# Kernel optimization log

Hardware: AMD Instinct MI355X
Metric: run time of the kernel (lower is better)

The kernel has to match this reference:

```python
import jax, jax.numpy as jnp
import numpy as np
import math

CH = 256
GROUPS = max(min(CH // 4, 32), 1)  # default_num_groups -> 32
EPS = 1e-5


def group_norm(x, gamma, beta):
    # x: [B, C, H, W]
    B, C, H, W = x.shape
    xg = x.reshape(B, GROUPS, C // GROUPS, H, W)
    mu = jnp.mean(xg, axis=(2, 3, 4), keepdims=True)
    var = jnp.var(xg, axis=(2, 3, 4), keepdims=True)
    xn = ((xg - mu) * jax.lax.rsqrt(var + EPS)).reshape(B, C, H, W)
    return xn * gamma[None, :, None, None] + beta[None, :, None, None]


def conv1x1(x, w, b):
    # x: [B, C_in, H, W]; w: [C_out, C_in]; b: [C_out]
    return jnp.einsum('oc,bchw->bohw', w, x) + b[None, :, None, None]


def xavier(key, shape, gain):
    fan_in, fan_out = shape[1], shape[0]
    limit = gain * math.sqrt(6.0 / (fan_in + fan_out))
    return jax.random.uniform(key, shape, jnp.float32, -limit, limit)


def setup_inputs() -> dict:
    key = jax.random.key(0)
    ks = jax.random.split(key, 6)
    x = jax.random.normal(ks[0], (32, CH, 32, 32), jnp.float32)
    gamma = jnp.ones((CH,), jnp.float32)
    beta = jnp.zeros((CH,), jnp.float32)
    g = math.sqrt(0.1)  # init_scale=0.1 for q,k,v
    wq = xavier(ks[1], (CH, CH), g)
    wk = xavier(ks[2], (CH, CH), g)
    wv = xavier(ks[3], (CH, CH), g)
    # w_h uses init_scale=0.0 -> zeros in original; use small nonzero so output is exercised
    wh = xavier(ks[4], (CH, CH), 0.1)
    bq = jnp.zeros((CH,), jnp.float32)
    bk = jnp.zeros((CH,), jnp.float32)
    bv = jnp.zeros((CH,), jnp.float32)
    bh = jnp.zeros((CH,), jnp.float32)
    return dict(x=x, gamma=gamma, beta=beta, wq=wq, bq=bq, wk=wk, bk=bk,
                wv=wv, bv=bv, wh=wh, bh=bh)


def reference(x, gamma, beta, wq, bq, wk, bk, wv, bv, wh, bh):
    B, C, H, W = x.shape
    N = H * W
    h = group_norm(x, gamma, beta)
    q = conv1x1(h, wq, bq).reshape(B, C, N)
    k = conv1x1(h, wk, bk).reshape(B, C, N)
    v = conv1x1(h, wv, bv).reshape(B, C, N)
    # full attention over spatial tokens: scores [B, N, N]
    scores = jnp.einsum('bcn,bcm->bnm', q, k) / math.sqrt(C)
    attn = jax.nn.softmax(scores, axis=-1)
    h = jnp.einsum('bnm,bcm->bcn', attn, v).reshape(B, C, H, W)
    h = conv1x1(h, wh, bh)
    return x + h  # skip_rescale=False
```

## Files before the change

kernel.cpp:

```cpp
#include <hip/hip_runtime.h>

typedef __bf16 bf16_t;
typedef __bf16 bf16x8 __attribute__((ext_vector_type(8)));
typedef __bf16 bf16x4 __attribute__((ext_vector_type(4)));
typedef float f32x4 __attribute__((ext_vector_type(4)));
typedef float f32x16 __attribute__((ext_vector_type(16)));
typedef long longx2 __attribute__((ext_vector_type(2)));
typedef unsigned uintx2 __attribute__((ext_vector_type(2)));

static constexpr int kC = 256;
static constexpr int kN = 1024;
static constexpr int kB = 32;

__device__ __forceinline__ void gload_lds16(const void* g, void* l) {
  __builtin_amdgcn_global_load_lds(
      (const __attribute__((address_space(1))) unsigned int*)g,
      (__attribute__((address_space(3))) unsigned int*)l, 16, 0, 0);
}

__device__ __forceinline__ unsigned pk_fp8x4(float a, float b, float c, float d) {
  unsigned r;
  asm("v_cvt_pk_fp8_f32 %0, %1, %2" : "=v"(r) : "v"(a), "v"(b));
  asm("v_cvt_pk_fp8_f32 %0, %1, %2 op_sel:[0,0,1]" : "+v"(r) : "v"(c), "v"(d));
  return r;
}

__device__ __forceinline__ void pl32swap(unsigned& a, unsigned& b) {
  asm("v_permlane32_swap_b32 %0, %1" : "+v"(a), "+v"(b));
}

__device__ __forceinline__ float cross_half_sum(float rs) {
  unsigned a = __builtin_bit_cast(unsigned, rs), b = a;
  pl32swap(a, b);
  return __builtin_bit_cast(float, a) + __builtin_bit_cast(float, b);
}

__global__ __launch_bounds__(256) void gn_castw_k(const float* __restrict__ x,
                                                  const float* __restrict__ gamma,
                                                  const float* __restrict__ beta,
                                                  bf16_t* __restrict__ hn,
                                                  const float* __restrict__ wq,
                                                  const float* __restrict__ wk,
                                                  const float* __restrict__ wv,
                                                  const float* __restrict__ wh,
                                                  bf16_t* __restrict__ wb) {
  __shared__ float xs[8 * 1040];
  __shared__ float red[8];
  __shared__ float stat[2];
  int t = threadIdx.x;
  if (blockIdx.x >= 1024) {
    int i = (blockIdx.x - 1024) * 256 + t;
    wb[i] = (bf16_t)wq[i];
    wb[i + 65536] = (bf16_t)wk[i];
    wb[i + 131072] = (bf16_t)wv[i];
    wb[i + 196608] = (bf16_t)wh[i];
    return;
  }
  int bg = blockIdx.x;
  int b = bg >> 5, g = bg & 31;
  const float* base = x + (size_t)bg * 8192;
  float s = 0.f, q = 0.f;
#pragma unroll
  for (int i = 0; i < 8; ++i) {
    float4 v = *(const float4*)(base + i * 1024 + t * 4);
    *(float4*)(xs + i * 1040 + t * 4) = v;
    s += v.x + v.y + v.z + v.w;
    q += v.x * v.x + v.y * v.y + v.z * v.z + v.w * v.w;
  }
#pragma unroll
  for (int o = 32; o; o >>= 1) { s += __shfl_down(s, o); q += __shfl_down(q, o); }
  int w = t >> 6;
  if ((t & 63) == 0) { red[w] = s; red[4 + w] = q; }
  __syncthreads();
  if (t == 0) {
    float S = red[0] + red[1] + red[2] + red[3];
    float Q = red[4] + red[5] + red[6] + red[7];
    float mean = S * (1.f / 8192.f);
    float var = Q * (1.f / 8192.f) - mean * mean;
    stat[0] = mean;
    stat[1] = rsqrtf(var + 1e-5f);
  }
  __syncthreads();
  float mean = stat[0], rstd = stat[1];
  float gmb[8], btb[8];
#pragma unroll
  for (int j = 0; j < 8; ++j) { gmb[j] = gamma[g * 8 + j]; btb[j] = beta[g * 8 + j]; }
  bf16_t* hb = hn + (size_t)b * (kN * kC) + g * 8;
#pragma unroll
  for (int i = 0; i < 4; ++i) {
    int n = i * 256 + t;
    bf16x8 o;
#pragma unroll
    for (int j = 0; j < 8; ++j)
      o[j] = (bf16_t)((xs[j * 1040 + n] - mean) * rstd * gmb[j] + btb[j]);
    *(bf16x8*)(hb + (size_t)n * kC) = o;
  }
}

__global__ __launch_bounds__(256, 2) void fattn_k(const char* __restrict__ QT,
                                                  const char* __restrict__ KT,
                                                  const char* __restrict__ VV,
                                                  bf16_t* __restrict__ OT) {
  __shared__ char smem[70656];
  char* lKc = smem;
  char* lVc = smem + 32768;
  char* pb = smem + 65536;
  float* exls = (float*)(smem + 69632);
  int t = threadIdx.x;
  int wid = t >> 6, lane = t & 63;
  int l31 = lane & 31, hi = lane >> 5;
  int qg = wid & 1, h = wid >> 1;
  int bid = blockIdx.x;
  int b = ((bid & 7) << 2) | ((bid >> 3) & 3);
  int qt = bid >> 5;
  const char* Qb = QT + (size_t)b * (kN * kC);
  int q0 = qt * 64 + qg * 32;
  constexpr float kSc = 0.0625f * 1.44269504f;

  long qf[16];
#pragma unroll
  for (int jj = 0; jj < 8; ++jj) {
    longx2 qp = *(const longx2*)(Qb + (size_t)(q0 + l31) * kC + hi * 128 + jj * 16);
    qf[2 * jj] = qp[0];
    qf[2 * jj + 1] = qp[1];
  }

  unsigned koff2[8];
#pragma unroll
  for (int jj = 0; jj < 8; ++jj)
    koff2[jj] = (h * 32 + l31) * 256 + (((hi * 8 + jj) ^ (l31 & 15)) << 4);
  unsigned voff2[8];
#pragma unroll
  for (int sp = 0; sp < 2; ++sp)
#pragma unroll
    for (int ct = 0; ct < 4; ++ct) {
      int c = h * 128 + ct * 32 + l31;
      voff2[sp * 4 + ct] = c * 64 + ((sp ^ ((c >> 1) & 1)) << 5) + hi * 16;
    }

  unsigned koffg[4], voffg[4];
#pragma unroll
  for (int i = 0; i < 4; ++i) {
    int ck = i * 256 + t;
    int row = ck >> 4, s = ck & 15;
    koffg[i] = row * 256 + ((s ^ (row & 15)) << 4);
    int cv = i * 256 + t;
    voffg[i] = (cv >> 2) * 1024 + ((cv & 3) << 4);
  }
  const char* kSrc = KT + (size_t)b * (kN * kC);
  const char* vSrc = VV + (size_t)b * (kC * kN);
  char* kd0 = lKc + t * 16;
  char* vd0 = lVc + t * 16;

  f32x16 acc[4] = {};
  float lsum = 0.f;

  auto STAGE = [&](int buf) {
#pragma unroll
    for (int i = 0; i < 4; ++i)
      gload_lds16(kSrc + koffg[i], kd0 + buf * 16384 + i * 4096);
#pragma unroll
    for (int i = 0; i < 4; ++i)
      gload_lds16(vSrc + voffg[i], vd0 + buf * 16384 + i * 4096);
    kSrc += 16384;
    vSrc += 64;
  };

  STAGE(0);
  for (int kt = 0; kt < 16; ++kt) {
    if (kt < 15) {
      STAGE((kt + 1) & 1);
      asm volatile("s_waitcnt vmcnt(8)" ::: "memory");
    } else {
      asm volatile("s_waitcnt vmcnt(0)" ::: "memory");
    }
    __builtin_amdgcn_s_barrier();
    const char* bK = lKc + (kt & 1) * 16384;
    const char* bV = lVc + (kt & 1) * 16384;
    f32x16 sa = {};
    __builtin_amdgcn_s_setprio(1);
#pragma unroll
    for (int jj = 0; jj < 8; ++jj) {
      longx2 ka = *(const longx2*)(bK + koff2[jj]);
      sa = __builtin_amdgcn_mfma_f32_32x32x16_fp8_fp8(ka[0], qf[2 * jj], sa, 0, 0, 0);
      sa = __builtin_amdgcn_mfma_f32_32x32x16_fp8_fp8(ka[1], qf[2 * jj + 1], sa, 0, 0, 0);
    }
    __builtin_amdgcn_s_setprio(0);
    float rs = 0.f;
    float e0 = exp2f(sa[0] * kSc), e1 = exp2f(sa[1] * kSc);
    float e2 = exp2f(sa[2] * kSc), e3 = exp2f(sa[3] * kSc);
    float e4 = exp2f(sa[4] * kSc), e5 = exp2f(sa[5] * kSc);
    float e6 = exp2f(sa[6] * kSc), e7 = exp2f(sa[7] * kSc);
    rs += e0 + e1 + e2 + e3 + e4 + e5 + e6 + e7;
    unsigned G0 = pk_fp8x4(e0, e1, e2, e3), G1 = pk_fp8x4(e4, e5, e6, e7);
    pl32swap(G0, G1);
    e0 = exp2f(sa[8] * kSc);  e1 = exp2f(sa[9] * kSc);
    e2 = exp2f(sa[10] * kSc); e3 = exp2f(sa[11] * kSc);
    e4 = exp2f(sa[12] * kSc); e5 = exp2f(sa[13] * kSc);
    e6 = exp2f(sa[14] * kSc); e7 = exp2f(sa[15] * kSc);
    rs += e0 + e1 + e2 + e3 + e4 + e5 + e6 + e7;
    lsum += rs;
    unsigned G2 = pk_fp8x4(e0, e1, e2, e3), G3 = pk_fp8x4(e4, e5, e6, e7);
    pl32swap(G2, G3);
    *(uint4*)(pb + wid * 1024 + lane * 16) = make_uint4(G0, G1, G2, G3);
    asm volatile("s_waitcnt lgkmcnt(0)" ::: "memory");
    __builtin_amdgcn_s_barrier();
    uint4 po = *(const uint4*)(pb + (wid ^ 2) * 1024 + lane * 16);
    long own0 = __builtin_bit_cast(long, uintx2{G0, G1});
    long own1 = __builtin_bit_cast(long, uintx2{G2, G3});
    long pr0 = __builtin_bit_cast(long, uintx2{po.x, po.y});
    long pr1 = __builtin_bit_cast(long, uintx2{po.z, po.w});
    long s0 = h ? pr0 : own0, s1 = h ? pr1 : own1;
    long s2 = h ? own0 : pr0, s3 = h ? own1 : pr1;
    __builtin_amdgcn_s_setprio(1);
#pragma unroll
    for (int ct = 0; ct < 4; ++ct) {
      longx2 vv = *(const longx2*)(bV + voff2[ct]);
      acc[ct] = __builtin_amdgcn_mfma_f32_32x32x16_fp8_fp8(s0, vv[0], acc[ct], 0, 0, 0);
      acc[ct] = __builtin_amdgcn_mfma_f32_32x32x16_fp8_fp8(s1, vv[1], acc[ct], 0, 0, 0);
    }
#pragma unroll
    for (int ct = 0; ct < 4; ++ct) {
      longx2 vv = *(const longx2*)(bV + voff2[4 + ct]);
      acc[ct] = __builtin_amdgcn_mfma_f32_32x32x16_fp8_fp8(s2, vv[0], acc[ct], 0, 0, 0);
      acc[ct] = __builtin_amdgcn_mfma_f32_32x32x16_fp8_fp8(s3, vv[1], acc[ct], 0, 0, 0);
    }
    __builtin_amdgcn_s_setprio(0);
    __builtin_amdgcn_s_barrier();
  }

  float ls = cross_half_sum(lsum);
  exls[wid * 64 + lane] = ls;
  __syncthreads();
  ls += exls[(wid ^ 2) * 64 + lane];
  float inv = 1.f / ls;
  float invR[16];
#pragma unroll
  for (int r = 0; r < 16; ++r)
    invR[r] = __shfl(inv, (r & 3) + 8 * (r >> 2) + 4 * hi);
  bf16_t* Ob = OT + (size_t)b * (kN * kC);
#pragma unroll
  for (int ct = 0; ct < 4; ++ct)
#pragma unroll
    for (int r = 0; r < 16; ++r) {
      int qr = (r & 3) + 8 * (r >> 2) + 4 * hi;
      Ob[(size_t)(q0 + qr) * kC + h * 128 + ct * 32 + l31] =
          (bf16_t)(acc[ct][r] * invR[r]);
    }
}

__global__ __launch_bounds__(256) void qkv_gemm_k(const bf16_t* __restrict__ W,
                                                  const bf16_t* __restrict__ HNall,
                                                  char* __restrict__ QTo,
                                                  char* __restrict__ KTo,
                                                  char* __restrict__ VVo,
                                                  const float* __restrict__ bq,
                                                  const float* __restrict__ bk,
                                                  const float* __restrict__ bv) {
  __shared__ bf16_t lA[2][128 * 64];
  __shared__ bf16_t lB[2][128 * 64];
  int bid = blockIdx.x;
  int b = bid / 48;
  int rem = bid - b * 48;
  int tmi = rem >> 3, tni = rem & 7;
  const bf16_t* Ab = W + (size_t)tmi * 128 * 256;
  const bf16_t* Bb = HNall + (size_t)b * (kN * kC) + (size_t)tni * 128 * 256;
  int t = threadIdx.x;
  int wid = t >> 6, l = t & 63;
  int wm = wid >> 1, wn = wid & 1;
  int lr = l & 15, lk = l >> 4;
  unsigned goff[4];
#pragma unroll
  for (int i = 0; i < 4; ++i) {
    int ci = i * 256 + t;
    int row = ci >> 3, s = ci & 7;
    goff[i] = row * 256 + ((s ^ (row & 7)) << 3);
  }
  unsigned aoff[8], boff[8];
#pragma unroll
  for (int kk = 0; kk < 2; ++kk)
#pragma unroll
    for (int f = 0; f < 4; ++f) {
      int ra = wm * 64 + f * 16 + lr;
      int rb2 = wn * 64 + f * 16 + lr;
      int ch = kk * 4 + lk;
      aoff[kk * 4 + f] = ra * 64 + ((ch ^ (ra & 7)) << 3);
      boff[kk * 4 + f] = rb2 * 64 + ((ch ^ (rb2 & 7)) << 3);
    }
  f32x4 acc[4][4] = {};
  auto STAGE = [&](int buf, int k0) {
#pragma unroll
    for (int i = 0; i < 4; ++i) {
      gload_lds16(Ab + k0 + goff[i], &lA[buf][t * 8 + i * 2048]);
      gload_lds16(Bb + k0 + goff[i], &lB[buf][t * 8 + i * 2048]);
    }
  };
  STAGE(0, 0);
  for (int kt = 0; kt < 4; ++kt) {
    if (kt < 3) {
      STAGE((kt + 1) & 1, (kt + 1) * 64);
      asm volatile("s_waitcnt vmcnt(8)" ::: "memory");
    } else {
      asm volatile("s_waitcnt vmcnt(0)" ::: "memory");
    }
    __builtin_amdgcn_s_barrier();
    const bf16_t* cA = lA[kt & 1];
    const bf16_t* cB = lB[kt & 1];
#pragma unroll
    for (int kk = 0; kk < 2; ++kk) {
      bf16x8 af[4], bfr[4];
#pragma unroll
      for (int f = 0; f < 4; ++f) {
        af[f] = *(const bf16x8*)(cA + aoff[kk * 4 + f]);
        bfr[f] = *(const bf16x8*)(cB + boff[kk * 4 + f]);
      }
#pragma unroll
      for (int mf = 0; mf < 4; ++mf)
#pragma unroll
        for (int nf = 0; nf < 4; ++nf)
          acc[mf][nf] = __builtin_amdgcn_mfma_f32_16x16x32_bf16(af[mf], bfr[nf],
                                                                acc[mf][nf], 0, 0, 0);
    }
    __builtin_amdgcn_s_barrier();
  }
  int seg = tmi >> 1;
  int rb = (tmi & 1) * 128 + wm * 64;
  int cb = tni * 128 + wn * 64;
  if (seg < 2) {
    char* D = (seg ? KTo : QTo) + (size_t)b * (kN * kC);
    const float* bias = seg ? bk : bq;
#pragma unroll
    for (int mf = 0; mf < 4; ++mf)
#pragma unroll
      for (int nf = 0; nf < 4; ++nf) {
        int r0 = rb + mf * 16 + lk * 4;
        int c = cb + nf * 16 + lr;
        unsigned u = pk_fp8x4(acc[mf][nf][0] + bias[r0], acc[mf][nf][1] + bias[r0 + 1],
                              acc[mf][nf][2] + bias[r0 + 2], acc[mf][nf][3] + bias[r0 + 3]);
        int np = ((r0 >> 3) & 1) * 128 + (r0 >> 4) * 8 + (r0 & 7);
        *(unsigned*)(D + (size_t)c * kC + np) = u;
      }
  } else {
    char* D = VVo + (size_t)b * (kC * kN);
#pragma unroll
    for (int mf = 0; mf < 4; ++mf)
#pragma unroll
      for (int nf = 0; nf < 4; ++nf) {
        int r0 = rb + mf * 16 + lk * 4;
        int c = cb + nf * 16 + lr;
        unsigned u = pk_fp8x4(acc[mf][nf][0] + bv[r0], acc[mf][nf][1] + bv[r0 + 1],
                              acc[mf][nf][2] + bv[r0 + 2], acc[mf][nf][3] + bv[r0 + 3]);
        int kv = c & 63, tile = c >> 6;
        int sp = kv >> 5;
        int base = tile * 64 + ((kv >> 3) & 1) * 16 + ((kv >> 4) & 1) * 8 + (kv & 7);
#pragma unroll
        for (int i = 0; i < 4; ++i) {
          int ch = r0 + i;
          int pos = base + ((sp ^ ((ch >> 1) & 1)) << 5);
          D[(size_t)ch * kN + pos] = (char)(u >> (8 * i));
        }
      }
  }
}

__global__ __launch_bounds__(256) void out_gemm_k(const bf16_t* __restrict__ A,
                                                  const bf16_t* __restrict__ BT,
                                                  float* __restrict__ Dst,
                                                  const float* __restrict__ bias,
                                                  const float* __restrict__ resid) {
  __shared__ bf16_t lA[2][128 * 64];
  __shared__ bf16_t lB[2][128 * 64];
  int bid = blockIdx.x;
  int b = bid >> 4;
  int rem = bid & 15;
  int tmi = rem >> 1, tni = rem & 1;
  const bf16_t* Ab = A + (size_t)b * (kN * kC) + (size_t)tmi * 128 * 256;
  const bf16_t* Bb = BT + (size_t)tni * 128 * 256;
  int t = threadIdx.x;
  int wid = t >> 6, l = t & 63;
  int wm = wid >> 1, wn = wid & 1;
  int lr = l & 15, lk = l >> 4;
  unsigned goff[4];
#pragma unroll
  for (int i = 0; i < 4; ++i) {
    int ci = i * 256 + t;
    int row = ci >> 3, s = ci & 7;
    goff[i] = row * 256 + ((s ^ (row & 7)) << 3);
  }
  unsigned aoff[8], boff[8];
#pragma unroll
  for (int kk = 0; kk < 2; ++kk)
#pragma unroll
    for (int f = 0; f < 4; ++f) {
      int ra = wm * 64 + f * 16 + lr;
      int rb2 = wn * 64 + f * 16 + lr;
      int ch = kk * 4 + lk;
      aoff[kk * 4 + f] = ra * 64 + ((ch ^ (ra & 7)) << 3);
      boff[kk * 4 + f] = rb2 * 64 + ((ch ^ (rb2 & 7)) << 3);
    }
  f32x4 acc[4][4] = {};
  auto STAGE = [&](int buf, int k0) {
#pragma unroll
    for (int i = 0; i < 4; ++i) {
      gload_lds16(Ab + k0 + goff[i], &lA[buf][t * 8 + i * 2048]);
      gload_lds16(Bb + k0 + goff[i], &lB[buf][t * 8 + i * 2048]);
    }
  };
  STAGE(0, 0);
  for (int kt = 0; kt < 4; ++kt) {
    if (kt < 3) {
      STAGE((kt + 1) & 1, (kt + 1) * 64);
      asm volatile("s_waitcnt vmcnt(8)" ::: "memory");
    } else {
      asm volatile("s_waitcnt vmcnt(0)" ::: "memory");
    }
    __builtin_amdgcn_s_barrier();
    const bf16_t* cA = lA[kt & 1];
    const bf16_t* cB = lB[kt & 1];
#pragma unroll
    for (int kk = 0; kk < 2; ++kk) {
      bf16x8 af[4], bfr[4];
#pragma unroll
      for (int f = 0; f < 4; ++f) {
        af[f] = *(const bf16x8*)(cA + aoff[kk * 4 + f]);
        bfr[f] = *(const bf16x8*)(cB + boff[kk * 4 + f]);
      }
#pragma unroll
      for (int mf = 0; mf < 4; ++mf)
#pragma unroll
        for (int nf = 0; nf < 4; ++nf)
          acc[mf][nf] = __builtin_amdgcn_mfma_f32_16x16x32_bf16(af[mf], bfr[nf],
                                                                acc[mf][nf], 0, 0, 0);
    }
    __builtin_amdgcn_s_barrier();
  }
  int rb = tmi * 128 + wm * 64;
  int cb = tni * 128 + wn * 64;
  float* D = Dst + (size_t)b * (kC * kN);
  const float* R = resid + (size_t)b * (kC * kN);
#pragma unroll
  for (int mf = 0; mf < 4; ++mf)
#pragma unroll
    for (int nf = 0; nf < 4; ++nf) {
      int r0 = rb + mf * 16 + lk * 4;
      int c = cb + nf * 16 + lr;
      float4 rv = *(const float4*)(R + (size_t)c * kN + r0);
      float bc = bias[c];
      float4 o2 = make_float4(acc[mf][nf][0] + rv.x + bc, acc[mf][nf][1] + rv.y + bc,
                              acc[mf][nf][2] + rv.z + bc, acc[mf][nf][3] + rv.w + bc);
      *(float4*)(D + (size_t)c * kN + r0) = o2;
    }
}

extern "C" void kernel_launch(void* const* d_in, const int* in_sizes, int n_in,
                              void* d_out, int out_size, void* d_ws, size_t ws_size,
                              hipStream_t stream) {
  (void)in_sizes; (void)n_in; (void)out_size; (void)ws_size;
  const float* x = (const float*)d_in[0];
  const float* gamma = (const float*)d_in[1];
  const float* beta = (const float*)d_in[2];
  const float* wq = (const float*)d_in[3];
  const float* bq = (const float*)d_in[4];
  const float* wk = (const float*)d_in[5];
  const float* bk = (const float*)d_in[6];
  const float* wv = (const float*)d_in[7];
  const float* bv = (const float*)d_in[8];
  const float* wh = (const float*)d_in[9];
  const float* bh = (const float*)d_in[10];
  float* out = (float*)d_out;

  char* ws = (char*)d_ws;
  bf16_t* HN = (bf16_t*)(ws);
  char* QT = ws + 16777216;
  char* KT = ws + 25165824;
  char* VV = ws + 33554432;
  bf16_t* WB = (bf16_t*)(ws + 50331648);

  gn_castw_k<<<kB * 32 + 256, 256, 0, stream>>>(x, gamma, beta, HN, wq, wk, wv, wh, WB);
  qkv_gemm_k<<<kB * 48, 256, 0, stream>>>(WB, HN, QT, KT, VV, bq, bk, bv);
  fattn_k<<<512, 256, 0, stream>>>(QT, KT, VV, HN);
  out_gemm_k<<<kB * 16, 256, 0, stream>>>(HN, WB + 196608, out, bh, x);
}
```

Baseline: 102.2 us.

## Keep activation tile resident in LDS and stream all QKV weight tiles

The QKV projection GEMM now loads a block's full 128x256 normalized-activation tile into LDS once. It then loops over all six 128-row weight tiles with double-buffered 64-wide K chunks, using 512 threads per block and 256 blocks instead of 1536. This removes the six-fold re-reading of the activation tile from global memory. The cost is a large LDS footprint (64KB plus the weight buffers), fewer blocks, and serialized epilogue stores inside the loop, which may lower occupancy and latency hiding.

```diff
diff --git a/kernel.cpp b/kernel.cpp
--- a/kernel.cpp
+++ b/kernel.cpp
@@ -249,7 +249,7 @@
     }
 }
 
-__global__ __launch_bounds__(256) void qkv_gemm_k(const bf16_t* __restrict__ W,
+__global__ __launch_bounds__(512) void qkv_gemm_k(const bf16_t* __restrict__ W,
                                                   const bf16_t* __restrict__ HNall,
                                                   char* __restrict__ QTo,
                                                   char* __restrict__ KTo,
@@ -257,109 +257,128 @@
                                                   const float* __restrict__ bq,
                                                   const float* __restrict__ bk,
                                                   const float* __restrict__ bv) {
-  __shared__ bf16_t lA[2][128 * 64];
-  __shared__ bf16_t lB[2][128 * 64];
+  __shared__ bf16_t lH[128 * 256];
+  __shared__ bf16_t lW[2][128 * 64];
   int bid = blockIdx.x;
-  int b = bid / 48;
-  int rem = bid - b * 48;
-  int tmi = rem >> 3, tni = rem & 7;
-  const bf16_t* Ab = W + (size_t)tmi * 128 * 256;
+  int b = bid >> 3, tni = bid & 7;
   const bf16_t* Bb = HNall + (size_t)b * (kN * kC) + (size_t)tni * 128 * 256;
   int t = threadIdx.x;
   int wid = t >> 6, l = t & 63;
   int wm = wid >> 1, wn = wid & 1;
   int lr = l & 15, lk = l >> 4;
-  unsigned goff[4];
-#pragma unroll
-  for (int i = 0; i < 4; ++i) {
-    int ci = i * 256 + t;
-    int row = ci >> 3, s = ci & 7;
-    goff[i] = row * 256 + ((s ^ (row & 7)) << 3);
-  }
-  unsigned aoff[8], boff[8];
+  unsigned hoff[8];
+#pragma unroll
+  for (int i = 0; i < 8; ++i) {
+    int d = i * 512 + t;
+    int row = d >> 5, sp = d & 31;
+    hoff[i] = row * 256 + ((sp ^ (row & 7)) << 3);
+  }
+  unsigned woff[2];
+#pragma unroll
+  for (int i = 0; i < 2; ++i) {
+    int d = i * 512 + t;
+    int row = d >> 3, sp = d & 7;
+    woff[i] = row * 256 + ((sp ^ (row & 7)) << 3);
+  }
+  unsigned aoff[2][8];
 #pragma unroll
   for (int kk = 0; kk < 2; ++kk)
 #pragma unroll
-    for (int f = 0; f < 4; ++f) {
-      int ra = wm * 64 + f * 16 + lr;
-      int rb2 = wn * 64 + f * 16 + lr;
+    for (int mf = 0; mf < 2; ++mf) {
+      int ra = wm * 32 + mf * 16 + lr;
       int ch = kk * 4 + lk;
-      aoff[kk * 4 + f] = ra * 64 + ((ch ^ (ra & 7)) << 3);
-      boff[kk * 4 + f] = rb2 * 64 + ((ch ^ (rb2 & 7)) << 3);
-    }
-  f32x4 acc[4][4] = {};
-  auto STAGE = [&](int buf, int k0) {
-#pragma unroll
-    for (int i = 0; i < 4; ++i) {
-      gload_lds16(Ab + k0 + goff[i], &lA[buf][t * 8 + i * 2048]);
-      gload_lds16(Bb + k0 + goff[i], &lB[buf][t * 8 + i * 2048]);
-    }
-  };
-  STAGE(0, 0);
-  for (int kt = 0; kt < 4; ++kt) {
-    if (kt < 3) {
-      STAGE((kt + 1) & 1, (kt + 1) * 64);
-      asm volatile("s_waitcnt vmcnt(8)" ::: "memory");
+      aoff[mf][kk] = ra * 64 + ((ch ^ (ra & 7)) << 3);
+    }
+  unsigned bofs[4];
+#pragma unroll
+  for (int nf = 0; nf < 4; ++nf) bofs[nf] = (unsigned)(wn * 64 + nf * 16 + lr);
+
+#pragma unroll
+  for (int i = 0; i < 8; ++i)
+    gload_lds16(Bb + hoff[i], lH + (size_t)(i * 512 + t) * 8);
+  const bf16_t* Wb = W;
+#pragma unroll
+  for (int i = 0; i < 2; ++i)
+    gload_lds16(Wb + woff[i], &lW[0][(i * 512 + t) * 8]);
+
+  f32x4 acc[2][4] = {};
+  for (int st = 0; st < 24; ++st) {
+    int tmi = st >> 2, ks = st & 3;
+    if (st < 23) {
+      int nst = st + 1;
+      const bf16_t* Wn = W + (size_t)(nst >> 2) * 128 * 256 + (nst & 3) * 64;
+#pragma unroll
+      for (int i = 0; i < 2; ++i)
+        gload_lds16(Wn + woff[i], &lW[nst & 1][(i * 512 + t) * 8]);
+      asm volatile("s_waitcnt vmcnt(2)" ::: "memory");
     } else {
       asm volatile("s_waitcnt vmcnt(0)" ::: "memory");
     }
     __builtin_amdgcn_s_barrier();
-    const bf16_t* cA = lA[kt & 1];
-    const bf16_t* cB = lB[kt & 1];
+    const bf16_t* cW = lW[st & 1];
 #pragma unroll
     for (int kk = 0; kk < 2; ++kk) {
-      bf16x8 af[4], bfr[4];
-#pragma unroll
-      for (int f = 0; f < 4; ++f) {
-        af[f] = *(const bf16x8*)(cA + aoff[kk * 4 + f]);
-        bfr[f] = *(const bf16x8*)(cB + boff[kk * 4 + f]);
+      bf16x8 af[2], bfr[4];
+#pragma unroll
+      for (int mf = 0; mf < 2; ++mf) af[mf] = *(const bf16x8*)(cW + aoff[mf][kk]);
+      int chh = ks * 8 + kk * 4 + lk;
+#pragma unroll
+      for (int nf = 0; nf < 4; ++nf) {
+        unsigned rb2 = bofs[nf];
+        bfr[nf] = *(const bf16x8*)(lH + rb2 * 256 + ((chh ^ (rb2 & 7)) << 3));
       }
 #pragma unroll
-      for (int mf = 0; mf < 4; ++mf)
+      for (int mf = 0; mf < 2; ++mf)
 #pragma unroll
         for (int nf = 0; nf < 4; ++nf)
           acc[mf][nf] = __builtin_amdgcn_mfma_f32_16x16x32_bf16(af[mf], bfr[nf],
                                                                 acc[mf][nf], 0, 0, 0);
     }
-    __builtin_amdgcn_s_barrier();
-  }
-  int seg = tmi >> 1;
-  int rb = (tmi & 1) * 128 + wm * 64;
-  int cb = tni * 128 + wn * 64;
-  if (seg < 2) {
-    char* D = (seg ? KTo : QTo) + (size_t)b * (kN * kC);
-    const float* bias = seg ? bk : bq;
-#pragma unroll
-    for (int mf = 0; mf < 4; ++mf)
-#pragma unroll
-      for (int nf = 0; nf < 4; ++nf) {
-        int r0 = rb + mf * 16 + lk * 4;
-        int c = cb + nf * 16 + lr;
-        unsigned u = pk_fp8x4(acc[mf][nf][0] + bias[r0], acc[mf][nf][1] + bias[r0 + 1],
-                              acc[mf][nf][2] + bias[r0 + 2], acc[mf][nf][3] + bias[r0 + 3]);
-        int np = ((r0 >> 3) & 1) * 128 + (r0 >> 4) * 8 + (r0 & 7);
-        *(unsigned*)(D + (size_t)c * kC + np) = u;
+    if (ks == 3) {
+      int seg = tmi >> 1;
+      int rbase = (tmi & 1) * 128 + wm * 32;
+      int cb = tni * 128 + wn * 64;
+      if (seg < 2) {
+        char* D = (seg ? KTo : QTo) + (size_t)b * (kN * kC);
+        const float* bias = seg ? bk : bq;
+#pragma unroll
+        for (int mf = 0; mf < 2; ++mf)
+#pragma unroll
+          for (int nf = 0; nf < 4; ++nf) {
+            int r0 = rbase + mf * 16 + lk * 4;
+            int c = cb + nf * 16 + lr;
+            unsigned u = pk_fp8x4(acc[mf][nf][0] + bias[r0], acc[mf][nf][1] + bias[r0 + 1],
+                                  acc[mf][nf][2] + bias[r0 + 2], acc[mf][nf][3] + bias[r0 + 3]);
+            int np = ((r0 >> 3) & 1) * 128 + (r0 >> 4) * 8 + (r0 & 7);
+            *(unsigned*)(D + (size_t)c * kC + np) = u;
+          }
+      } else {
+        char* D = VVo + (size_t)b * (kC * kN);
+#pragma unroll
+        for (int mf = 0; mf < 2; ++mf)
+#pragma unroll
+          for (int nf = 0; nf < 4; ++nf) {
+            int r0 = rbase + mf * 16 + lk * 4;
+            int c = cb + nf * 16 + lr;
+            unsigned u = pk_fp8x4(acc[mf][nf][0] + bv[r0], acc[mf][nf][1] + bv[r0 + 1],
+                                  acc[mf][nf][2] + bv[r0 + 2], acc[mf][nf][3] + bv[r0 + 3]);
+            int kv = c & 63, tile = c >> 6;
+            int sp = kv >> 5;
+            int base = tile * 64 + ((kv >> 3) & 1) * 16 + ((kv >> 4) & 1) * 8 + (kv & 7);
+#pragma unroll
+            for (int i = 0; i < 4; ++i) {
+              int ch = r0 + i;
+              int pos = base + ((sp ^ ((ch >> 1) & 1)) << 5);
+              D[(size_t)ch * kN + pos] = (char)(u >> (8 * i));
+            }
+          }
       }
-  } else {
-    char* D = VVo + (size_t)b * (kC * kN);
-#pragma unroll
-    for (int mf = 0; mf < 4; ++mf)
-#pragma unroll
-      for (int nf = 0; nf < 4; ++nf) {
-        int r0 = rb + mf * 16 + lk * 4;
-        int c = cb + nf * 16 + lr;
-        unsigned u = pk_fp8x4(acc[mf][nf][0] + bv[r0], acc[mf][nf][1] + bv[r0 + 1],
-                              acc[mf][nf][2] + bv[r0 + 2], acc[mf][nf][3] + bv[r0 + 3]);
-        int kv = c & 63, tile = c >> 6;
-        int sp = kv >> 5;
-        int base = tile * 64 + ((kv >> 3) & 1) * 16 + ((kv >> 4) & 1) * 8 + (kv & 7);
-#pragma unroll
-        for (int i = 0; i < 4; ++i) {
-          int ch = r0 + i;
-          int pos = base + ((sp ^ ((ch >> 1) & 1)) << 5);
-          D[(size_t)ch * kN + pos] = (char)(u >> (8 * i));
-        }
-      }
+#pragma unroll
+      for (int mf = 0; mf < 2; ++mf)
+#pragma unroll
+        for (int nf = 0; nf < 4; ++nf) acc[mf][nf] = f32x4{0.f, 0.f, 0.f, 0.f};
+    }
+    __builtin_amdgcn_s_barrier();
   }
 }
 
@@ -477,7 +496,7 @@
   bf16_t* WB = (bf16_t*)(ws + 50331648);
 
   gn_castw_k<<<kB * 32 + 256, 256, 0, stream>>>(x, gamma, beta, HN, wq, wk, wv, wh, WB);
-  qkv_gemm_k<<<kB * 48, 256, 0, stream>>>(WB, HN, QT, KT, VV, bq, bk, bv);
+  qkv_gemm_k<<<kB * 8, 512, 0, stream>>>(WB, HN, QT, KT, VV, bq, bk, bv);
   fattn_k<<<512, 256, 0, stream>>>(QT, KT, VV, HN);
   out_gemm_k<<<kB * 16, 256, 0, stream>>>(HN, WB + 196608, out, bh, x);
 }
```

Result: slower. 110.8 us (+8.4%).
